# Optimization experiments

Measured on AMD Instinct MI355X. Metric: run time of the kernel, lower is better.

## Reference

```python
import jax, jax.numpy as jnp
import numpy as np

B, T, DM, H, HD = 2, 2048, 1024, 16, 64

def _rope_cos_sin(t, hd):
    inv_freq = 1.0 / (10000.0 ** (jnp.arange(0, hd, 2, dtype=jnp.float32) / hd))
    ang = jnp.arange(t, dtype=jnp.float32)[:, None] * inv_freq[None, :]  # [T, hd/2]
    emb = jnp.concatenate([ang, ang], axis=-1)  # [T, hd]
    return jnp.cos(emb), jnp.sin(emb)

def setup_inputs() -> dict:
    key = jax.random.key(0)
    kx, kq, kp = jax.random.split(key, 3)
    x = jax.random.normal(kx, (B, T, DM), dtype=jnp.float32)
    cos, sin = _rope_cos_sin(T, HD)
    w_qkv = jax.random.normal(kq, (3 * DM, DM), dtype=jnp.float32) * (DM ** -0.5)
    w_proj = jax.random.normal(kp, (DM, DM), dtype=jnp.float32) * (DM ** -0.5)
    return {"x": x, "cos": cos, "sin": sin, "w_qkv": w_qkv, "w_proj": w_proj}

def _rotate_half(u):
    d = u.shape[-1] // 2
    return jnp.concatenate([-u[..., d:], u[..., :d]], axis=-1)

def _apply_rope(u, cos, sin):
    # u: [B, T, H, D]; cos/sin: [T, D] -> unsqueeze_dim=1 -> [T, 1, D]
    c = cos[:, None, :]
    s = sin[:, None, :]
    return u * c + _rotate_half(u) * s

def reference(x, cos, sin, w_qkv, w_proj):
    b, t, _ = x.shape
    qkv = jnp.einsum('btd,ed->bte', x, w_qkv)            # [B, T, 3*DM]
    qkv = qkv.reshape(b, t, 3, H, HD)
    q, k, v = qkv[:, :, 0], qkv[:, :, 1], qkv[:, :, 2]   # each [B, T, H, HD]
    q = _apply_rope(q, cos, sin)
    k = _apply_rope(k, cos, sin)
    q = q.transpose(0, 2, 1, 3)                          # [B, H, T, HD]
    k = k.transpose(0, 2, 1, 3)
    v = v.transpose(0, 2, 1, 3)
    scale = 1.0 / jnp.sqrt(jnp.float32(HD))
    scores = jnp.einsum('bhqd,bhkd->bhqk', q, k) * scale  # [B, H, T, T]
    causal = jnp.tril(jnp.ones((t, t), dtype=bool))
    scores = jnp.where(causal[None, None], scores, jnp.finfo(scores.dtype).min)
    attn = jax.nn.softmax(scores, axis=-1)
    out = jnp.einsum('bhqk,bhkd->bhqd', attn, v)          # [B, H, T, HD]
    out = out.transpose(0, 2, 1, 3).reshape(b, t, H * HD)
    return jnp.einsum('btd,ed->bte', out, w_proj)
```

## Files before the change

kernel.cpp:

```cpp
#include <hip/hip_runtime.h>
#include <stdint.h>

#define Bb 2
#define Tt 2048
#define DMm 1024
#define Hh 16
#define HDd 64
#define Mrows (Bb*Tt)

typedef __attribute__((ext_vector_type(8)))  __bf16 bf16x8;
typedef __attribute__((ext_vector_type(4)))  __bf16 bf16x4;
typedef __attribute__((ext_vector_type(4)))  float  f32x4;
typedef __attribute__((ext_vector_type(16))) float  f32x16;
typedef __attribute__((ext_vector_type(4)))  unsigned int u32x4;
typedef __attribute__((ext_vector_type(2)))  unsigned int u32x2;

#define GLD16(gp, lp) __builtin_amdgcn_global_load_lds( \
    (const __attribute__((address_space(1))) unsigned int*)(gp), \
    (__attribute__((address_space(3))) unsigned int*)(lp), 16, 0, 0)

static __device__ __forceinline__ unsigned cvtpk_bf16(float lo, float hi) {
  unsigned r;
  asm("v_cvt_pk_bf16_f32 %0, %1, %2" : "=v"(r) : "v"(lo), "v"(hi));
  return r;
}
static __device__ __forceinline__ float exp2_hw(float x) {
  float r;
  asm("v_exp_f32 %0, %1" : "=v"(r) : "v"(x));
  return r;
}
static __device__ __forceinline__ float fmax3(float a, float b, float c) {
  return fmaxf(fmaxf(a, b), c);
}
static __device__ __forceinline__ float xmax32(float v) {
  return fmaxf(v, __shfl_xor(v, 32));
}
static __device__ __forceinline__ float xsum32(float v) {
  return v + __shfl_xor(v, 32);
}

__global__ __launch_bounds__(256)
void cast3_k(const float* __restrict__ a, const float* __restrict__ b,
             const float* __restrict__ c,
             __bf16* __restrict__ oa, __bf16* __restrict__ ob,
             __bf16* __restrict__ oc,
             const float* __restrict__ cosb, const float* __restrict__ sinb,
             unsigned* __restrict__ cs) {
  const int NA = 1048576, NB = 786432, NC = 262144;
  int i = blockIdx.x * 256 + threadIdx.x;
  if (i < NA + NB + NC) {
    const float* src; __bf16* dst; int k;
    if (i < NA)            { src = a; dst = oa; k = i; }
    else if (i < NA + NB)  { src = b; dst = ob; k = i - NA; }
    else                   { src = c; dst = oc; k = i - NA - NB; }
    float4 v = ((const float4*)src)[k];
    bf16x4 o;
    o[0] = (__bf16)v.x; o[1] = (__bf16)v.y; o[2] = (__bf16)v.z; o[3] = (__bf16)v.w;
    ((bf16x4*)dst)[k] = o;
  } else {
    int k = i - (NA + NB + NC);
    cs[k] = cvtpk_bf16(cosb[k], sinb[k]);
  }
}

__global__ __launch_bounds__(256)
void gemm_bt(const __bf16* __restrict__ A, const __bf16* __restrict__ Bm,
             float* __restrict__ C) {
  const int N = 1024, K = 1024;
  __shared__ __bf16 As[128 * 32];
  __shared__ __bf16 Bs[64 * 32];
  const int bid = blockIdx.x;
  const int xcd = bid & 7, i2 = bid >> 3;
  const int rowBase = (xcd * 4 + (i2 & 3)) * 128;
  const int colBase = (i2 >> 2) * 64;
  const int tid  = threadIdx.x;
  const int lane = tid & 63, wid = tid >> 6;
  const int l4 = lane & 15, lhi = lane >> 4;
  const int wh = wid >> 1, ww = wid & 1;
  f32x4 acc[4][2] = {};
  const int e0 = wid * 512 + lane * 8;
  const int r0 = e0 >> 5, c0 = e0 & 31;
  const __bf16* a0 = A  + (size_t)(rowBase + r0)      * K + c0;
  const __bf16* a1 = A  + (size_t)(rowBase + r0 + 64) * K + c0;
  const __bf16* b0 = Bm + (size_t)(colBase + r0)      * K + c0;
  for (int k0 = 0; k0 < K; k0 += 32) {
    __syncthreads();
    GLD16(a0 + k0, &As[wid * 512]);
    GLD16(a1 + k0, &As[2048 + wid * 512]);
    GLD16(b0 + k0, &Bs[wid * 512]);
    __syncthreads();
    bf16x8 af[4], bfr[2];
#pragma unroll
    for (int i = 0; i < 4; i++)
      af[i]  = *(const bf16x8*)&As[(wh * 64 + i * 16 + l4) * 32 + lhi * 8];
#pragma unroll
    for (int j = 0; j < 2; j++)
      bfr[j] = *(const bf16x8*)&Bs[(ww * 32 + j * 16 + l4) * 32 + lhi * 8];
#pragma unroll
    for (int i = 0; i < 4; i++)
#pragma unroll
      for (int j = 0; j < 2; j++)
        acc[i][j] = __builtin_amdgcn_mfma_f32_16x16x32_bf16(af[i], bfr[j], acc[i][j], 0, 0, 0);
  }
#pragma unroll
  for (int i = 0; i < 4; i++) {
    int R = rowBase + wh * 64 + i * 16 + lhi * 4;
#pragma unroll
    for (int j = 0; j < 2; j++) {
      int Cc = colBase + ww * 32 + j * 16 + l4;
      float* cp = C + (size_t)R * N + Cc;
#pragma unroll
      for (int q = 0; q < 4; q++) cp[(size_t)q * N] = acc[i][j][q];
    }
  }
}

__global__ __launch_bounds__(256)
void gemm_qkv(const __bf16* __restrict__ A, const __bf16* __restrict__ Bm,
              __bf16* __restrict__ Qb, __bf16* __restrict__ Kb,
              __bf16* __restrict__ Vfb, const unsigned* __restrict__ csb) {
  const int K = 1024;
  __shared__ __bf16 ldsu[16384];
  __bf16* As = ldsu;
  __bf16* Bs = ldsu + 4096;
  const int bid = blockIdx.x;
  const int xcd = bid & 7, i2 = bid >> 3;
  const int rowBase = (xcd * 4 + (i2 & 3)) * 128;
  const int colBase = (i2 >> 2) * 128;
  const int tid  = threadIdx.x;
  const int lane = tid & 63, wid = tid >> 6;
  const int l4 = lane & 15, lhi = lane >> 4;
  const int wh = wid >> 1, ww = wid & 1;
  f32x4 acc[4][4] = {};
  const int e0 = wid * 512 + lane * 8;
  const int r0 = e0 >> 5, c0 = e0 & 31;
  const __bf16* a0 = A  + (size_t)(rowBase + r0)      * K + c0;
  const __bf16* a1 = A  + (size_t)(rowBase + r0 + 64) * K + c0;
  const __bf16* b0 = Bm + (size_t)(colBase + r0)      * K + c0;
  const __bf16* b1 = Bm + (size_t)(colBase + r0 + 64) * K + c0;
  for (int k0 = 0; k0 < K; k0 += 32) {
    __syncthreads();
    GLD16(a0 + k0, &As[wid * 512]);
    GLD16(a1 + k0, &As[2048 + wid * 512]);
    GLD16(b0 + k0, &Bs[wid * 512]);
    GLD16(b1 + k0, &Bs[2048 + wid * 512]);
    __syncthreads();
    bf16x8 af[4], bfr[4];
#pragma unroll
    for (int i = 0; i < 4; i++) {
      af[i]  = *(const bf16x8*)&As[(wh * 64 + i * 16 + l4) * 32 + lhi * 8];
      bfr[i] = *(const bf16x8*)&Bs[(ww * 64 + i * 16 + l4) * 32 + lhi * 8];
    }
#pragma unroll
    for (int i = 0; i < 4; i++)
#pragma unroll
      for (int j = 0; j < 4; j++)
        acc[i][j] = __builtin_amdgcn_mfma_f32_16x16x32_bf16(af[i], bfr[j], acc[i][j], 0, 0, 0);
  }

  const int region = colBase >> 10;
  const int base_h = (colBase & 1023) >> 6;
  const int bIdx   = rowBase >> 11;
  const int tileBase = (rowBase & 2047) >> 5;

  __syncthreads();

  if (region < 2) {
    const float qscale = region ? 1.f : 0.18033688f;
#pragma unroll
    for (int i = 0; i < 4; i++) {
      const int tbase = ww * 8192 + (wh * 2 + (i >> 1)) * 2048;
      const int rsub  = (i & 1) * 16 + lhi * 4;
      const int trow0 = (rowBase & 2047) + wh * 64 + i * 16 + lhi * 4;
#pragma unroll
      for (int j = 0; j < 4; j++) {
        int dd = j * 16 + l4;
        float sg = (j < 2) ? -1.f : 1.f;
        int lbase = tbase + j * 512 + (l4 >> 3) * 256 + (l4 & 7);
#pragma unroll
        for (int q = 0; q < 4; q++) {
          unsigned cw = csb[(trow0 + q) * 64 + dd];
          float cc = __builtin_bit_cast(float, cw << 16);
          float sn = __builtin_bit_cast(float, cw & 0xffff0000u);
          float r = (acc[i][j][q] * cc + sg * acc[i][j ^ 2][q] * sn) * qscale;
          ldsu[lbase + (rsub + q) * 8] = (__bf16)r;
        }
      }
    }
  } else {
#pragma unroll
    for (int i = 0; i < 4; i++) {
      const int tbase = ww * 8192 + (wh * 2 + (i >> 1)) * 2048 + (i & 1) * 512;
#pragma unroll
      for (int j = 0; j < 4; j++) {
        int lbase = tbase + (j >> 1) * 1024 + ((j & 1) * 16 + l4) * 8;
#pragma unroll
        for (int q = 0; q < 4; q++) {
          int rq = lhi * 4 + q;
          ldsu[lbase + ((rq >> 3) & 1) * 256 + (rq & 7)] = (__bf16)acc[i][j][q];
        }
      }
    }
  }
  __syncthreads();

  __bf16* dstBuf = (region == 0) ? Qb : (region == 1 ? Kb : Vfb);
#pragma unroll
  for (int h2 = 0; h2 < 2; ++h2) {
    __bf16* dst = dstBuf + (size_t)(bIdx * 16 + base_h + h2) * (Tt * 64)
                + (size_t)tileBase * 2048;
#pragma unroll
    for (int k = 0; k < 4; ++k) {
      int eoff = k * 2048 + tid * 8;
      *(bf16x8*)(dst + eoff) = *(const bf16x8*)&ldsu[h2 * 8192 + eoff];
    }
  }
}

__global__ __launch_bounds__(256)
void attn_k(const __bf16* __restrict__ Q, const __bf16* __restrict__ K,
            const __bf16* __restrict__ Vb, __bf16* __restrict__ O) {
  const int bid = blockIdx.x;
  const int xcd = bid & 7;
  const int ii  = bid >> 3;
  const int bh  = xcd * 4 + (ii & 3);
  const int jj  = ii >> 2;
  const int b = bh >> 4, h = bh & 15;
  const int tid = threadIdx.x, lane = tid & 63, w = tid >> 6;
  const int l5 = lane & 31, hi = lane >> 5;
  const size_t baseF = (size_t)bh * (Tt * 64);
  const int laneoff = (hi << 8) + (l5 << 3);
  const float NEG_INF = -__builtin_inff();

  __shared__ float  oL[4][32][65];
  __shared__ float2 msL[4][32];

#define FRAGP(P, tile, c) ((P) + baseF + (size_t)(((tile) * 4 + (c)) << 9) + laneoff)

#define LOADK(KA, TIX) do {                                               \
    KA[0] = *(const bf16x8*)FRAGP(K, (TIX), 0);                           \
    KA[1] = *(const bf16x8*)FRAGP(K, (TIX), 1);                           \
    KA[2] = *(const bf16x8*)FRAGP(K, (TIX), 2);                           \
    KA[3] = *(const bf16x8*)FRAGP(K, (TIX), 3);                           \
  } while (0)
#define LOADV(TIX) do {                                                   \
    vc[0] = *(const bf16x8*)FRAGP(Vb, (TIX), 0);                          \
    vc[1] = *(const bf16x8*)FRAGP(Vb, (TIX), 1);                          \
    vc[2] = *(const bf16x8*)FRAGP(Vb, (TIX), 2);                          \
    vc[3] = *(const bf16x8*)FRAGP(Vb, (TIX), 3);                          \
  } while (0)

#define COMPUTE(KA, TIX) do {                                             \
    f32x16 s = {};                                                        \
    __builtin_amdgcn_s_setprio(1);                                        \
    s = __builtin_amdgcn_mfma_f32_32x32x16_bf16(KA[0], qf[0], s, 0, 0, 0);\
    s = __builtin_amdgcn_mfma_f32_32x32x16_bf16(KA[1], qf[1], s, 0, 0, 0);\
    s = __builtin_amdgcn_mfma_f32_32x32x16_bf16(KA[2], qf[2], s, 0, 0, 0);\
    s = __builtin_amdgcn_mfma_f32_32x32x16_bf16(KA[3], qf[3], s, 0, 0, 0);\
    __builtin_amdgcn_s_setprio(0);                                        \
    if ((TIX) == qsub) {                                                  \
      _Pragma("unroll")                                                   \
      for (int r = 0; r < 16; r++) {                                      \
        int kof = (r & 3) + 8 * (r >> 2) + 4 * hi;                        \
        s[r] = (kof <= l5) ? s[r] : NEG_INF;                              \
      }                                                                   \
    }                                                                     \
    float t0 = fmax3(s[0], s[1], s[2]);                                   \
    float t1 = fmax3(s[3], s[4], s[5]);                                   \
    float t2 = fmax3(s[6], s[7], s[8]);                                   \
    float t3 = fmax3(s[9], s[10], s[11]);                                 \
    float t4 = fmax3(s[12], s[13], s[14]);                                \
    float pmax = fmaxf(fmax3(t0, t1, t2), fmax3(t3, t4, s[15]));          \
    pmax = xmax32(pmax);                                                  \
    if (__any(pmax > m + 11.5f)) {                                        \
      float mn = fmaxf(m, pmax);                                          \
      float al = exp2_hw(m - mn);                                         \
      m = mn;                                                             \
      ssum *= al;                                                         \
      float arow[16];                                                     \
      _Pragma("unroll")                                                   \
      for (int r = 0; r < 16; r++)                                        \
        arow[r] = __shfl(al, (r & 3) + 8 * (r >> 2) + 4 * hi);            \
      _Pragma("unroll")                                                   \
      for (int r = 0; r < 16; r++) { o0[r] *= arow[r]; o1[r] *= arow[r]; }\
    }                                                                     \
    float p[16], rsl = 0.f;                                               \
    _Pragma("unroll")                                                     \
    for (int r = 0; r < 16; r++) { p[r] = exp2_hw(s[r] - m); rsl += p[r]; } \
    ssum += xsum32(rsl);                                                  \
    bf16x8 pa[2];                                                         \
    _Pragma("unroll")                                                     \
    for (int kc = 0; kc < 2; kc++) {                                      \
      const float* pp = p + kc * 8;                                       \
      unsigned X0 = cvtpk_bf16(pp[0], pp[1]);                             \
      unsigned Y0 = cvtpk_bf16(pp[4], pp[5]);                             \
      unsigned X1 = cvtpk_bf16(pp[2], pp[3]);                             \
      unsigned Y1 = cvtpk_bf16(pp[6], pp[7]);                             \
      u32x2 q0 = __builtin_amdgcn_permlane32_swap(X0, Y0, false, false);  \
      u32x2 q1 = __builtin_amdgcn_permlane32_swap(X1, Y1, false, false);  \
      u32x4 pw;                                                           \
      pw[0] = q0[0]; pw[1] = q1[0]; pw[2] = q0[1]; pw[3] = q1[1];         \
      pa[kc] = __builtin_bit_cast(bf16x8, pw);                            \
    }                                                                     \
    __builtin_amdgcn_s_setprio(1);                                        \
    o0 = __builtin_amdgcn_mfma_f32_32x32x16_bf16(pa[0], vc[0], o0, 0, 0, 0);\
    o0 = __builtin_amdgcn_mfma_f32_32x32x16_bf16(pa[1], vc[1], o0, 0, 0, 0);\
    o1 = __builtin_amdgcn_mfma_f32_32x32x16_bf16(pa[0], vc[2], o1, 0, 0, 0);\
    o1 = __builtin_amdgcn_mfma_f32_32x32x16_bf16(pa[1], vc[3], o1, 0, 0, 0);\
    __builtin_amdgcn_s_setprio(0);                                        \
  } while (0)

#define TCLAMP(tx) ( ((tx) > qsub) ? qsub : (tx) )

  for (int ph = 0; ph < 2; ++ph) {
    const int qsub  = ph ? (63 - jj) : jj;
    const int qrow0 = qsub * 32;

    bf16x8 qf[4];
#pragma unroll
    for (int cc = 0; cc < 4; cc++)
      qf[cc] = *(const bf16x8*)FRAGP(Q, qsub, cc);

    f32x16 o0 = {}, o1 = {};
    float m = NEG_INF, ssum = 0.f;

    const int NT = qsub + 1;
    const int dtw = NT - w;
    const int n = (dtw > 0) ? ((dtw + 3) >> 2) : 0;

    bf16x8 kA[4], kB[4], vc[4];

    LOADK(kA, TCLAMP(w));
    int i = 0;
    for (; i + 2 <= n; i += 2) {
      LOADV(w + 4 * i);
      LOADK(kB, TCLAMP(w + 4 * i + 4));
      COMPUTE(kA, w + 4 * i);
      LOADV(w + 4 * i + 4);
      LOADK(kA, TCLAMP(w + 4 * i + 8));
      COMPUTE(kB, w + 4 * i + 4);
    }
    if (i < n) {
      LOADV(w + 4 * i);
      COMPUTE(kA, w + 4 * i);
    }

#pragma unroll
    for (int r = 0; r < 16; r++) {
      int row = (r & 3) + 8 * (r >> 2) + 4 * hi;
      oL[w][row][l5]      = o0[r];
      oL[w][row][32 + l5] = o1[r];
    }
    if (hi == 0) msL[w][l5] = make_float2(m, ssum);
    __syncthreads();

    {
      const int row = l5;
      const int dbase = w * 16 + hi * 8;
      float2 s0 = msL[0][row], s1 = msL[1][row], s2 = msL[2][row], s3 = msL[3][row];
      float M = fmaxf(fmaxf(s0.x, s1.x), fmaxf(s2.x, s3.x));
      float a0 = exp2_hw(s0.x - M), a1 = exp2_hw(s1.x - M);
      float a2 = exp2_hw(s2.x - M), a3 = exp2_hw(s3.x - M);
      float inv = 1.f / (a0 * s0.y + a1 * s1.y + a2 * s2.y + a3 * s3.y);
      bf16x8 ov;
#pragma unroll
      for (int e = 0; e < 8; e++) {
        float v = a0 * oL[0][row][dbase + e] + a1 * oL[1][row][dbase + e]
                + a2 * oL[2][row][dbase + e] + a3 * oL[3][row][dbase + e];
        ov[e] = (__bf16)(v * inv);
      }
      *(bf16x8*)(O + ((size_t)b * Tt + qrow0 + row) * DMm + h * 64 + dbase) = ov;
    }
    __syncthreads();
  }
}

extern "C" void kernel_launch(void* const* d_in, const int* in_sizes, int n_in,
                              void* d_out, int out_size, void* d_ws, size_t ws_size,
                              hipStream_t stream) {
  const float* x     = (const float*)d_in[0];
  const float* cosb  = (const float*)d_in[1];
  const float* sinb  = (const float*)d_in[2];
  const float* wqkv  = (const float*)d_in[3];
  const float* wproj = (const float*)d_in[4];
  float* out = (float*)d_out;

  char* ws = (char*)d_ws;
  __bf16*   xb     = (__bf16*)(ws + 0);
  __bf16*   wqkvb  = (__bf16*)(ws + 8388608);
  __bf16*   wprojb = (__bf16*)(ws + 14680064);
  unsigned* csb    = (unsigned*)(ws + 16777216);
  __bf16*   Qb     = (__bf16*)(ws + 17825792);
  __bf16*   Kb     = (__bf16*)(ws + 26214400);
  __bf16*   Vfb    = (__bf16*)(ws + 34603008);
  __bf16*   attno  = (__bf16*)(ws + 42991616);

  cast3_k<<<8704, 256, 0, stream>>>(x, wqkv, wproj, xb, wqkvb, wprojb,
                                    cosb, sinb, csb);

  gemm_qkv<<<768, 256, 0, stream>>>(xb, wqkvb, Qb, Kb, Vfb, csb);

  attn_k<<<1024, 256, 0, stream>>>(Qb, Kb, Vfb, attno);

  gemm_bt<<<512, 256, 0, stream>>>(attno, wprojb, out);
}
```

Before: 99.19 us.

## Fuse x cast into QKV GEMM and split attention into one tile per block

The cast of x to bf16 moves out of the cast kernel and into the QKV GEMM, which now stages fp32 x tiles in LDS with a swizzled layout and converts them to bf16 when forming fragments. This drops one full write and re-read of x, but the GEMM moves twice as many A bytes per tile and uses double the LDS. The attention kernel no longer pairs a short and a long query tile per block: it launches 2048 blocks of one tile each, longest tiles first, with a launch-bounds occupancy hint. It merges the output in two halves through a smaller LDS buffer to cut shared memory, at the cost of losing the built-in load balancing and adding an extra barrier.

```diff
diff --git a/kernel.cpp b/kernel.cpp
--- a/kernel.cpp
+++ b/kernel.cpp
@@ -40,25 +40,22 @@
 }
 
 __global__ __launch_bounds__(256)
-void cast3_k(const float* __restrict__ a, const float* __restrict__ b,
-             const float* __restrict__ c,
-             __bf16* __restrict__ oa, __bf16* __restrict__ ob,
-             __bf16* __restrict__ oc,
+void cast3_k(const float* __restrict__ b, const float* __restrict__ c,
+             __bf16* __restrict__ ob, __bf16* __restrict__ oc,
              const float* __restrict__ cosb, const float* __restrict__ sinb,
              unsigned* __restrict__ cs) {
-  const int NA = 1048576, NB = 786432, NC = 262144;
+  const int NB = 786432, NC = 262144;
   int i = blockIdx.x * 256 + threadIdx.x;
-  if (i < NA + NB + NC) {
+  if (i < NB + NC) {
     const float* src; __bf16* dst; int k;
-    if (i < NA)            { src = a; dst = oa; k = i; }
-    else if (i < NA + NB)  { src = b; dst = ob; k = i - NA; }
-    else                   { src = c; dst = oc; k = i - NA - NB; }
+    if (i < NB) { src = b; dst = ob; k = i; }
+    else        { src = c; dst = oc; k = i - NB; }
     float4 v = ((const float4*)src)[k];
     bf16x4 o;
     o[0] = (__bf16)v.x; o[1] = (__bf16)v.y; o[2] = (__bf16)v.z; o[3] = (__bf16)v.w;
     ((bf16x4*)dst)[k] = o;
   } else {
-    int k = i - (NA + NB + NC);
+    int k = i - (NB + NC);
     cs[k] = cvtpk_bf16(cosb[k], sinb[k]);
   }
 }
@@ -116,13 +113,14 @@
 }
 
 __global__ __launch_bounds__(256)
-void gemm_qkv(const __bf16* __restrict__ A, const __bf16* __restrict__ Bm,
+void gemm_qkv(const float* __restrict__ X, const __bf16* __restrict__ Bm,
               __bf16* __restrict__ Qb, __bf16* __restrict__ Kb,
               __bf16* __restrict__ Vfb, const unsigned* __restrict__ csb) {
   const int K = 1024;
-  __shared__ __bf16 ldsu[16384];
-  __bf16* As = ldsu;
-  __bf16* Bs = ldsu + 4096;
+  __shared__ __align__(16) char lds_raw[32768];
+  float*  Asf   = (float*)lds_raw;
+  __bf16* Bsh   = (__bf16*)(lds_raw + 16384);
+  __bf16* stage = (__bf16*)lds_raw;
   const int bid = blockIdx.x;
   const int xcd = bid & 7, i2 = bid >> 3;
   const int rowBase = (xcd * 4 + (i2 & 3)) * 128;
@@ -132,24 +130,37 @@
   const int l4 = lane & 15, lhi = lane >> 4;
   const int wh = wid >> 1, ww = wid & 1;
   f32x4 acc[4][4] = {};
+
+  const int arow = wid * 8 + (lane >> 3);
+  const int acol = ((lane & 7) ^ ((lane >> 3) & 7)) * 4;
+  const float* a0f = X + (size_t)(rowBase + arow) * K + acol;
+
   const int e0 = wid * 512 + lane * 8;
   const int r0 = e0 >> 5, c0 = e0 & 31;
-  const __bf16* a0 = A  + (size_t)(rowBase + r0)      * K + c0;
-  const __bf16* a1 = A  + (size_t)(rowBase + r0 + 64) * K + c0;
   const __bf16* b0 = Bm + (size_t)(colBase + r0)      * K + c0;
   const __bf16* b1 = Bm + (size_t)(colBase + r0 + 64) * K + c0;
+
   for (int k0 = 0; k0 < K; k0 += 32) {
     __syncthreads();
-    GLD16(a0 + k0, &As[wid * 512]);
-    GLD16(a1 + k0, &As[2048 + wid * 512]);
-    GLD16(b0 + k0, &Bs[wid * 512]);
-    GLD16(b1 + k0, &Bs[2048 + wid * 512]);
+    GLD16(a0f + k0,            &Asf[wid * 256]);
+    GLD16(a0f + 32 * K + k0,   &Asf[1024 + wid * 256]);
+    GLD16(a0f + 64 * K + k0,   &Asf[2048 + wid * 256]);
+    GLD16(a0f + 96 * K + k0,   &Asf[3072 + wid * 256]);
+    GLD16(b0 + k0, &Bsh[wid * 512]);
+    GLD16(b1 + k0, &Bsh[2048 + wid * 512]);
     __syncthreads();
     bf16x8 af[4], bfr[4];
+    const int k7 = l4 & 7;
 #pragma unroll
     for (int i = 0; i < 4; i++) {
-      af[i]  = *(const bf16x8*)&As[(wh * 64 + i * 16 + l4) * 32 + lhi * 8];
-      bfr[i] = *(const bf16x8*)&Bs[(ww * 64 + i * 16 + l4) * 32 + lhi * 8];
+      const float* ap = &Asf[(wh * 64 + i * 16 + l4) * 32];
+      f32x4 fa = *(const f32x4*)(ap + (((2 * lhi)     ^ k7) * 4));
+      f32x4 fb = *(const f32x4*)(ap + (((2 * lhi + 1) ^ k7) * 4));
+      u32x4 aw;
+      aw[0] = cvtpk_bf16(fa[0], fa[1]); aw[1] = cvtpk_bf16(fa[2], fa[3]);
+      aw[2] = cvtpk_bf16(fb[0], fb[1]); aw[3] = cvtpk_bf16(fb[2], fb[3]);
+      af[i]  = __builtin_bit_cast(bf16x8, aw);
+      bfr[i] = *(const bf16x8*)&Bsh[(ww * 64 + i * 16 + l4) * 32 + lhi * 8];
     }
 #pragma unroll
     for (int i = 0; i < 4; i++)
@@ -183,7 +194,7 @@
           float cc = __builtin_bit_cast(float, cw << 16);
           float sn = __builtin_bit_cast(float, cw & 0xffff0000u);
           float r = (acc[i][j][q] * cc + sg * acc[i][j ^ 2][q] * sn) * qscale;
-          ldsu[lbase + (rsub + q) * 8] = (__bf16)r;
+          stage[lbase + (rsub + q) * 8] = (__bf16)r;
         }
       }
     }
@@ -197,7 +208,7 @@
 #pragma unroll
         for (int q = 0; q < 4; q++) {
           int rq = lhi * 4 + q;
-          ldsu[lbase + ((rq >> 3) & 1) * 256 + (rq & 7)] = (__bf16)acc[i][j][q];
+          stage[lbase + ((rq >> 3) & 1) * 256 + (rq & 7)] = (__bf16)acc[i][j][q];
         }
       }
     }
@@ -212,27 +223,28 @@
 #pragma unroll
     for (int k = 0; k < 4; ++k) {
       int eoff = k * 2048 + tid * 8;
-      *(bf16x8*)(dst + eoff) = *(const bf16x8*)&ldsu[h2 * 8192 + eoff];
-    }
-  }
-}
-
-__global__ __launch_bounds__(256)
+      *(bf16x8*)(dst + eoff) = *(const bf16x8*)&stage[h2 * 8192 + eoff];
+    }
+  }
+}
+
+__global__ __launch_bounds__(256, 5)
 void attn_k(const __bf16* __restrict__ Q, const __bf16* __restrict__ K,
             const __bf16* __restrict__ Vb, __bf16* __restrict__ O) {
   const int bid = blockIdx.x;
   const int xcd = bid & 7;
   const int ii  = bid >> 3;
   const int bh  = xcd * 4 + (ii & 3);
-  const int jj  = ii >> 2;
+  const int qsub = 63 - (ii >> 2);
   const int b = bh >> 4, h = bh & 15;
   const int tid = threadIdx.x, lane = tid & 63, w = tid >> 6;
   const int l5 = lane & 31, hi = lane >> 5;
+  const int qrow0 = qsub * 32;
   const size_t baseF = (size_t)bh * (Tt * 64);
   const int laneoff = (hi << 8) + (l5 << 3);
   const float NEG_INF = -__builtin_inff();
 
-  __shared__ float  oL[4][32][65];
+  __shared__ float  oL2[4][32][33];
   __shared__ float2 msL[4][32];
 
 #define FRAGP(P, tile, c) ((P) + baseF + (size_t)(((tile) * 4 + (c)) << 9) + laneoff)
@@ -312,66 +324,80 @@
 
 #define TCLAMP(tx) ( ((tx) > qsub) ? qsub : (tx) )
 
-  for (int ph = 0; ph < 2; ++ph) {
-    const int qsub  = ph ? (63 - jj) : jj;
-    const int qrow0 = qsub * 32;
-
-    bf16x8 qf[4];
-#pragma unroll
-    for (int cc = 0; cc < 4; cc++)
-      qf[cc] = *(const bf16x8*)FRAGP(Q, qsub, cc);
-
-    f32x16 o0 = {}, o1 = {};
-    float m = NEG_INF, ssum = 0.f;
-
-    const int NT = qsub + 1;
-    const int dtw = NT - w;
-    const int n = (dtw > 0) ? ((dtw + 3) >> 2) : 0;
-
-    bf16x8 kA[4], kB[4], vc[4];
-
-    LOADK(kA, TCLAMP(w));
-    int i = 0;
-    for (; i + 2 <= n; i += 2) {
-      LOADV(w + 4 * i);
-      LOADK(kB, TCLAMP(w + 4 * i + 4));
-      COMPUTE(kA, w + 4 * i);
-      LOADV(w + 4 * i + 4);
-      LOADK(kA, TCLAMP(w + 4 * i + 8));
-      COMPUTE(kB, w + 4 * i + 4);
-    }
-    if (i < n) {
-      LOADV(w + 4 * i);
-      COMPUTE(kA, w + 4 * i);
-    }
-
-#pragma unroll
-    for (int r = 0; r < 16; r++) {
-      int row = (r & 3) + 8 * (r >> 2) + 4 * hi;
-      oL[w][row][l5]      = o0[r];
-      oL[w][row][32 + l5] = o1[r];
-    }
-    if (hi == 0) msL[w][l5] = make_float2(m, ssum);
-    __syncthreads();
-
-    {
-      const int row = l5;
-      const int dbase = w * 16 + hi * 8;
-      float2 s0 = msL[0][row], s1 = msL[1][row], s2 = msL[2][row], s3 = msL[3][row];
-      float M = fmaxf(fmaxf(s0.x, s1.x), fmaxf(s2.x, s3.x));
-      float a0 = exp2_hw(s0.x - M), a1 = exp2_hw(s1.x - M);
-      float a2 = exp2_hw(s2.x - M), a3 = exp2_hw(s3.x - M);
-      float inv = 1.f / (a0 * s0.y + a1 * s1.y + a2 * s2.y + a3 * s3.y);
-      bf16x8 ov;
-#pragma unroll
-      for (int e = 0; e < 8; e++) {
-        float v = a0 * oL[0][row][dbase + e] + a1 * oL[1][row][dbase + e]
-                + a2 * oL[2][row][dbase + e] + a3 * oL[3][row][dbase + e];
-        ov[e] = (__bf16)(v * inv);
-      }
-      *(bf16x8*)(O + ((size_t)b * Tt + qrow0 + row) * DMm + h * 64 + dbase) = ov;
-    }
-    __syncthreads();
+  bf16x8 qf[4];
+#pragma unroll
+  for (int cc = 0; cc < 4; cc++)
+    qf[cc] = *(const bf16x8*)FRAGP(Q, qsub, cc);
+
+  f32x16 o0 = {}, o1 = {};
+  float m = NEG_INF, ssum = 0.f;
+
+  const int NT = qsub + 1;
+  const int dtw = NT - w;
+  const int n = (dtw > 0) ? ((dtw + 3) >> 2) : 0;
+
+  bf16x8 kA[4], kB[4], vc[4];
+
+  LOADK(kA, TCLAMP(w));
+  int i = 0;
+  for (; i + 2 <= n; i += 2) {
+    LOADV(w + 4 * i);
+    LOADK(kB, TCLAMP(w + 4 * i + 4));
+    COMPUTE(kA, w + 4 * i);
+    LOADV(w + 4 * i + 4);
+    LOADK(kA, TCLAMP(w + 4 * i + 8));
+    COMPUTE(kB, w + 4 * i + 4);
+  }
+  if (i < n) {
+    LOADV(w + 4 * i);
+    COMPUTE(kA, w + 4 * i);
+  }
+
+#pragma unroll
+  for (int r = 0; r < 16; r++) {
+    int wrow = (r & 3) + 8 * (r >> 2) + 4 * hi;
+    oL2[w][wrow][l5] = o0[r];
+  }
+  if (hi == 0) msL[w][l5] = make_float2(m, ssum);
+  __syncthreads();
+
+  const int row = l5;
+  const int cb  = w * 8 + hi * 4;
+  float2 s0 = msL[0][row], s1 = msL[1][row], s2 = msL[2][row], s3 = msL[3][row];
+  float M = fmaxf(fmaxf(s0.x, s1.x), fmaxf(s2.x, s3.x));
+  float a0 = exp2_hw(s0.x - M), a1 = exp2_hw(s1.x - M);
+  float a2 = exp2_hw(s2.x - M), a3 = exp2_hw(s3.x - M);
+  float inv = 1.f / (a0 * s0.y + a1 * s1.y + a2 * s2.y + a3 * s3.y);
+  __bf16* orow = O + ((size_t)b * Tt + qrow0 + row) * DMm + h * 64;
+
+  {
+    bf16x4 ov;
+#pragma unroll
+    for (int e = 0; e < 4; e++) {
+      float v = a0 * oL2[0][row][cb + e] + a1 * oL2[1][row][cb + e]
+              + a2 * oL2[2][row][cb + e] + a3 * oL2[3][row][cb + e];
+      ov[e] = (__bf16)(v * inv);
+    }
+    *(bf16x4*)(orow + cb) = ov;
+  }
+  __syncthreads();
+
+#pragma unroll
+  for (int r = 0; r < 16; r++) {
+    int wrow = (r & 3) + 8 * (r >> 2) + 4 * hi;
+    oL2[w][wrow][l5] = o1[r];
+  }
+  __syncthreads();
+
+  {
+    bf16x4 ov;
+#pragma unroll
+    for (int e = 0; e < 4; e++) {
+      float v = a0 * oL2[0][row][cb + e] + a1 * oL2[1][row][cb + e]
+              + a2 * oL2[2][row][cb + e] + a3 * oL2[3][row][cb + e];
+      ov[e] = (__bf16)(v * inv);
+    }
+    *(bf16x4*)(orow + 32 + cb) = ov;
   }
 }
 
@@ -386,21 +412,20 @@
   float* out = (float*)d_out;
 
   char* ws = (char*)d_ws;
-  __bf16*   xb     = (__bf16*)(ws + 0);
-  __bf16*   wqkvb  = (__bf16*)(ws + 8388608);
-  __bf16*   wprojb = (__bf16*)(ws + 14680064);
-  unsigned* csb    = (unsigned*)(ws + 16777216);
-  __bf16*   Qb     = (__bf16*)(ws + 17825792);
-  __bf16*   Kb     = (__bf16*)(ws + 26214400);
-  __bf16*   Vfb    = (__bf16*)(ws + 34603008);
-  __bf16*   attno  = (__bf16*)(ws + 42991616);
-
-  cast3_k<<<8704, 256, 0, stream>>>(x, wqkv, wproj, xb, wqkvb, wprojb,
+  __bf16*   wqkvb  = (__bf16*)(ws + 0);
+  __bf16*   wprojb = (__bf16*)(ws + 6291456);
+  unsigned* csb    = (unsigned*)(ws + 8388608);
+  __bf16*   Qb     = (__bf16*)(ws + 9437184);
+  __bf16*   Kb     = (__bf16*)(ws + 17825792);
+  __bf16*   Vfb    = (__bf16*)(ws + 26214400);
+  __bf16*   attno  = (__bf16*)(ws + 34603008);
+
+  cast3_k<<<4608, 256, 0, stream>>>(wqkv, wproj, wqkvb, wprojb,
                                     cosb, sinb, csb);
 
-  gemm_qkv<<<768, 256, 0, stream>>>(xb, wqkvb, Qb, Kb, Vfb, csb);
-
-  attn_k<<<1024, 256, 0, stream>>>(Qb, Kb, Vfb, attno);
+  gemm_qkv<<<768, 256, 0, stream>>>(x, wqkvb, Qb, Kb, Vfb, csb);
+
+  attn_k<<<2048, 256, 0, stream>>>(Qb, Kb, Vfb, attno);
 
   gemm_bt<<<512, 256, 0, stream>>>(attno, wprojb, out);
 }
```

Result: slower. 225.7 us (+127.6%).
